# Performance work log

Measured on AMD Instinct MI355X. Metric: run time of the kernel, lower is better.

The kernel has to match this reference:

```python
import jax, jax.numpy as jnp
import numpy as np

B, N, D, H = 1024, 128, 256, 8
DH = D // H
CLIP = 10.0   # tanh clipping of logits (Kool attention model default)
NEG = -1e9    # mask value


def setup_inputs() -> dict:
    key = jax.random.key(0)
    ks = jax.random.split(key, 12)
    s = 1.0 / np.sqrt(D)
    rn = lambda k, shape, sc: jax.random.normal(k, shape, dtype=jnp.float32) * sc
    return {
        'coords': jax.random.uniform(ks[0], (B, N, 2), dtype=jnp.float32),
        'embeddings': rn(ks[1], (B, N, D), 1.0),
        'Wk': rn(ks[2], (D, D), s),            # glimpse key projection
        'Wv': rn(ks[3], (D, D), s),            # glimpse value projection
        'Wlk': rn(ks[4], (D, D), s),           # logit key projection
        'Wo': rn(ks[5], (D, D), s),            # glimpse output projection
        'Wc': rn(ks[6], (D, D), s),            # project_fixed_context
        'Ws': rn(ks[7], (2 * D, D), s),        # project_step_context (concat first,prev)
        'W_placeholder': rn(ks[8], (2 * D,), 1.0),  # first-step context placeholder
        'W1': rn(ks[9], (D, D), s),            # new_weight_1 (xavier-ish)
        'b1': jnp.zeros((D,), jnp.float32),    # new_bias_1 (init 0)
        'W2': jnp.zeros((D, D), jnp.float32),  # new_weight_2 (init 0 -> identity residual)
        'b2': jnp.zeros((D,), jnp.float32),    # new_bias_2 (init 0)
    }


def _decode(embeddings, Wk, Wv, Wlk, Wo, Wc, Ws, W_placeholder, W1, b1, W2, b2):
    Bq, Nq, Dq = embeddings.shape
    # precompute attention node data (fixed across steps)
    Kh = (embeddings @ Wk).reshape(Bq, Nq, H, DH).transpose(0, 2, 1, 3)  # [B,H,N,DH]
    Vh = (embeddings @ Wv).reshape(Bq, Nq, H, DH).transpose(0, 2, 1, 3)  # [B,H,N,DH]
    logitK = embeddings @ Wlk                                            # [B,N,D]
    glimpse0 = embeddings.mean(1)                                        # [B,D]
    visited0 = jnp.zeros((Bq, Nq), dtype=bool)
    idx0 = jnp.zeros((Bq,), dtype=jnp.int32)

    def body(carry, step):
        visited, first, prev, glimpse = carry
        first_emb = jnp.take_along_axis(embeddings, first[:, None, None], axis=1)[:, 0]
        prev_emb = jnp.take_along_axis(embeddings, prev[:, None, None], axis=1)[:, 0]
        step_ctx = jnp.where(step == 0,
                             jnp.broadcast_to(W_placeholder, (Bq, 2 * Dq)),
                             jnp.concatenate([first_emb, prev_emb], axis=-1))
        # query = graph context (updated glimpse) + step context
        q = glimpse @ Wc + step_ctx @ Ws                                  # [B,D]
        # query_transform: residual 2-layer MLP
        q = q + (jax.nn.relu(q @ W1 + b1) @ W2 + b2)
        # one_to_many_logits: MHA glimpse, then single-head pointer logits
        qh = q.reshape(Bq, H, DH)
        compat = jnp.einsum('bhd,bhnd->bhn', qh, Kh) / np.sqrt(DH)
        compat = jnp.where(visited[:, None, :], NEG, compat)
        attn = jax.nn.softmax(compat, axis=-1)
        heads = jnp.einsum('bhn,bhnd->bhd', attn, Vh).reshape(Bq, Dq)
        new_glimpse = heads @ Wo                                          # [B,D]
        logits = jnp.einsum('bd,bnd->bn', new_glimpse, logitK) / np.sqrt(Dq)
        logits = CLIP * jnp.tanh(logits)
        logits = jnp.where(visited, NEG, logits)
        log_p = jax.nn.log_softmax(logits, axis=-1)                       # [B,N]
        sel = jnp.argmax(log_p, axis=-1).astype(jnp.int32)                # greedy select
        visited = visited | jax.nn.one_hot(sel, Nq, dtype=bool)
        first = jnp.where(step == 0, sel, first)
        return (visited, first, sel, new_glimpse), (log_p, sel)

    _, (log_ps, sels) = jax.lax.scan(body, (visited0, idx0, idx0, glimpse0),
                                     jnp.arange(Nq))
    return log_ps.transpose(1, 0, 2), sels.transpose(1, 0)  # [B,steps,N], [B,steps]


def _tour_cost(coords, pi):
    route = jnp.take_along_axis(coords, pi[:, :, None].astype(jnp.int32), axis=1)  # [B,N,2]
    diffs = route - jnp.roll(route, -1, axis=1)
    return jnp.sqrt((diffs * diffs).sum(-1)).sum(-1)  # [B]


def reference(coords, embeddings, Wk, Wv, Wlk, Wo, Wc, Ws, W_placeholder, W1, b1, W2, b2):
    log_ps, pi = _decode(embeddings, Wk, Wv, Wlk, Wo, Wc, Ws, W_placeholder, W1, b1, W2, b2)
    cost = _tour_cost(coords, pi)
    ll = jnp.take_along_axis(log_ps, pi[:, :, None], axis=2)[:, :, 0].sum(-1)  # [B]
    return cost, ll
```

## Files before the change

kernel.cpp:

```cpp
#include <hip/hip_runtime.h>
#include <math.h>


#define BB 1024
#define NN 128
#define DD 256
#define HH 8

__device__ __forceinline__ float4 f4z() { return make_float4(0.f, 0.f, 0.f, 0.f); }
__device__ __forceinline__ float4 f4fma(float4 a, float4 b, float4 c) {
  c.x = fmaf(a.x, b.x, c.x); c.y = fmaf(a.y, b.y, c.y);
  c.z = fmaf(a.z, b.z, c.z); c.w = fmaf(a.w, b.w, c.w); return c;
}
__device__ __forceinline__ float4 svfma(float s, float4 w, float4 c) {
  c.x = fmaf(s, w.x, c.x); c.y = fmaf(s, w.y, c.y);
  c.z = fmaf(s, w.z, c.z); c.w = fmaf(s, w.w, c.w); return c;
}
__device__ __forceinline__ float4 f4scale(float4 a, float s) {
  a.x *= s; a.y *= s; a.z *= s; a.w *= s; return a;
}

#define WAVE_SYNC() do { asm volatile("s_waitcnt lgkmcnt(0)" ::: "memory"); \
                         __builtin_amdgcn_sched_barrier(0); } while (0)

__global__ void k_mean(const float* __restrict__ E, float* __restrict__ g0) {
  int b = blockIdx.x, t = threadIdx.x;
  const float* e = E + (size_t)b * NN * DD + t;
  float s = 0.f;
#pragma unroll 8
  for (int n = 0; n < NN; ++n) s += e[n * DD];
  g0[b * DD + t] = s * (1.f / 128.f);
}

__global__ void k_transpose(const float* __restrict__ A, float* __restrict__ AT) {
  __shared__ float tile[32][33];
  int bi = blockIdx.x & 7, bo = blockIdx.x >> 3;
  int tx = threadIdx.x & 31, ty = threadIdx.x >> 5;
  for (int j = 0; j < 32; j += 8)
    tile[ty + j][tx] = A[(size_t)(bi * 32 + ty + j) * DD + bo * 32 + tx];
  __syncthreads();
  for (int j = 0; j < 32; j += 8)
    AT[(size_t)(bo * 32 + ty + j) * DD + bi * 32 + tx] = tile[tx][ty + j];
}

__global__ __launch_bounds__(256) void k_gemm(const float* __restrict__ A,
                                              const float* __restrict__ Bm,
                                              float* __restrict__ C,
                                              int M, int Nn, int K, int transB) {
  __shared__ float As[32][33], Bs[32][33];
  int tn = blockIdx.x, tm = blockIdx.y;
  int t = threadIdx.x;
  int c = t & 31, r4 = t >> 5;
  float acc[4] = {0.f, 0.f, 0.f, 0.f};
  for (int k0 = 0; k0 < K; k0 += 32) {
#pragma unroll
    for (int i = 0; i < 4; ++i) {
      int li = t + i * 256; int ar = li >> 5, ac = li & 31;
      As[ar][ac] = A[(size_t)(tm * 32 + ar) * K + k0 + ac];
    }
    if (!transB) {
#pragma unroll
      for (int i = 0; i < 4; ++i) {
        int li = t + i * 256; int kk = li >> 5, cc = li & 31;
        Bs[kk][cc] = Bm[(size_t)(k0 + kk) * Nn + tn * 32 + cc];
      }
    } else {
#pragma unroll
      for (int i = 0; i < 4; ++i) {
        int li = t + i * 256; int cc = li >> 5, kk = li & 31;
        Bs[kk][cc] = Bm[(size_t)(tn * 32 + cc) * K + k0 + kk];
      }
    }
    __syncthreads();
#pragma unroll
    for (int kk = 0; kk < 32; ++kk) {
      float bv = Bs[kk][c];
#pragma unroll
      for (int i = 0; i < 4; ++i) acc[i] += As[r4 + i * 8][kk] * bv;
    }
    __syncthreads();
  }
#pragma unroll
  for (int i = 0; i < 4; ++i)
    C[(size_t)(tm * 32 + r4 + i * 8) * Nn + tn * 32 + c] = acc[i];
}

__global__ __launch_bounds__(512, 2) void k_decode(
    const float* __restrict__ E, const float* __restrict__ coords,
    const float* __restrict__ Ws, const float* __restrict__ W1,
    const float* __restrict__ b1, const float* __restrict__ W2,
    const float* __restrict__ b2, const float* __restrict__ WkT,
    const float* __restrict__ Wv, const float* __restrict__ M1,
    const float* __restrict__ M2, const float* __restrict__ Wph,
    const float* __restrict__ qlin0, float* __restrict__ out) {
  __shared__ float ctxS[512 * 4];
  __shared__ float qS[256 * 4];
  __shared__ float hS[256 * 4];
  __shared__ float q2S[256 * 4];
  __shared__ float headsS[256 * 4];
  __shared__ float qkS[8320];
  __shared__ float hEnS[8320];
  __shared__ float qlinS[4][256];
  __shared__ float gl2S[4][256];
  __shared__ float plS[4 * 2 * 8 * 8];
  __shared__ float alS[4 * 2 * 8];
  __shared__ float mlS[4 * 2 * 8 * 2];
  __shared__ int   lstS[4][128];
  __shared__ float logitS[4][128];
  __shared__ unsigned visS[4][4];
  __shared__ int   fpS[4][2];
  __shared__ float stS[4][8];

  const int t = threadIdx.x;
  const int w = t >> 6, l = t & 63;
  const int blk = blockIdx.x;
  const int ks = w;
  const int c0 = l * 4;
  const int fbb = w >> 1, w2 = w & 1;

  if (t < 256) {
    int bb = t >> 6, cc = (t & 63) * 4;
    *(float4*)&qlinS[bb][cc] =
        *(const float4*)(qlin0 + (size_t)(blk * 4 + bb) * DD + cc);
  }
  if (t < 16) visS[t >> 2][t & 3] = 0u;
  if (t < 4) {
    fpS[t][0] = 0; fpS[t][1] = 0;
#pragma unroll
    for (int j = 0; j < 8; ++j) stS[t][j] = 0.f;
  }
  __syncthreads();

  for (int step = 0; step < NN; ++step) {
    const int cnt = NN - step;

    if (step == 0) {
      float v = Wph[t];
      *(float4*)&ctxS[t * 4] = make_float4(v, v, v, v);
    } else {
      int bb = t >> 7, i4 = (t & 127) * 4;
      int node = (i4 < 256) ? fpS[bb][0] : fpS[bb][1];
      float4 v = *(const float4*)(E + (size_t)(blk * 4 + bb) * (NN * DD) +
                                  (size_t)node * DD + (i4 & 255));
      ctxS[(i4 + 0) * 4 + bb] = v.x; ctxS[(i4 + 1) * 4 + bb] = v.y;
      ctxS[(i4 + 2) * 4 + bb] = v.z; ctxS[(i4 + 3) * 4 + bb] = v.w;
    }
    __syncthreads();

    {
      float4 a0 = f4z(), a1 = f4z(), a2 = f4z(), a3 = f4z();
      const float* wp = Ws + (size_t)(ks * 64) * DD + c0;
      const float* cp = ctxS + (ks * 64) * 4;
#pragma unroll 8
      for (int k = 0; k < 64; ++k) {
        float4 wv = *(const float4*)wp; wp += DD;
        float4 cv = *(const float4*)cp; cp += 4;
        a0 = svfma(cv.x, wv, a0); a1 = svfma(cv.y, wv, a1);
        a2 = svfma(cv.z, wv, a2); a3 = svfma(cv.w, wv, a3);
      }
      *(float4*)&hEnS[ks * 1024 + 0 * 256 + c0] = a0;
      *(float4*)&hEnS[ks * 1024 + 1 * 256 + c0] = a1;
      *(float4*)&hEnS[ks * 1024 + 2 * 256 + c0] = a2;
      *(float4*)&hEnS[ks * 1024 + 3 * 256 + c0] = a3;
    }
    __syncthreads();
    {
      int bb = t & 3, cb = t >> 2;
#pragma unroll
      for (int it = 0; it < 2; ++it) {
        int c = cb + it * 128;
        float s = qlinS[bb][c];
#pragma unroll
        for (int sl = 0; sl < 8; ++sl) s += hEnS[sl * 1024 + bb * 256 + c];
        qS[c * 4 + bb] = s;
      }
    }
    __syncthreads();

    {
      float4 a0 = f4z(), a1 = f4z(), a2 = f4z(), a3 = f4z();
      const float* wp = W1 + (size_t)(ks * 32) * DD + c0;
      const float* qp = qS + (ks * 32) * 4;
#pragma unroll 8
      for (int k = 0; k < 32; ++k) {
        float4 wv = *(const float4*)wp; wp += DD;
        float4 qv = *(const float4*)qp; qp += 4;
        a0 = svfma(qv.x, wv, a0); a1 = svfma(qv.y, wv, a1);
        a2 = svfma(qv.z, wv, a2); a3 = svfma(qv.w, wv, a3);
      }
      *(float4*)&hEnS[ks * 1024 + 0 * 256 + c0] = a0;
      *(float4*)&hEnS[ks * 1024 + 1 * 256 + c0] = a1;
      *(float4*)&hEnS[ks * 1024 + 2 * 256 + c0] = a2;
      *(float4*)&hEnS[ks * 1024 + 3 * 256 + c0] = a3;
    }
    __syncthreads();
    {
      int bb = t & 3, cb = t >> 2;
#pragma unroll
      for (int it = 0; it < 2; ++it) {
        int c = cb + it * 128;
        float s = b1[c];
#pragma unroll
        for (int sl = 0; sl < 8; ++sl) s += hEnS[sl * 1024 + bb * 256 + c];
        hS[c * 4 + bb] = fmaxf(s, 0.f);
      }
    }
    __syncthreads();

    {
      float4 a0 = f4z(), a1 = f4z(), a2 = f4z(), a3 = f4z();
      const float* wp = W2 + (size_t)(ks * 32) * DD + c0;
      const float* hp = hS + (ks * 32) * 4;
#pragma unroll 8
      for (int k = 0; k < 32; ++k) {
        float4 wv = *(const float4*)wp; wp += DD;
        float4 hv = *(const float4*)hp; hp += 4;
        a0 = svfma(hv.x, wv, a0); a1 = svfma(hv.y, wv, a1);
        a2 = svfma(hv.z, wv, a2); a3 = svfma(hv.w, wv, a3);
      }
      *(float4*)&hEnS[ks * 1024 + 0 * 256 + c0] = a0;
      *(float4*)&hEnS[ks * 1024 + 1 * 256 + c0] = a1;
      *(float4*)&hEnS[ks * 1024 + 2 * 256 + c0] = a2;
      *(float4*)&hEnS[ks * 1024 + 3 * 256 + c0] = a3;
    }
    __syncthreads();
    {
      int bb = t & 3, cb = t >> 2;
#pragma unroll
      for (int it = 0; it < 2; ++it) {
        int c = cb + it * 128;
        float s = qS[c * 4 + bb] + b2[c];
#pragma unroll
        for (int sl = 0; sl < 8; ++sl) s += hEnS[sl * 1024 + bb * 256 + c];
        q2S[c * 4 + bb] = s;
      }
    }
    __syncthreads();

    {
      const int h = w;
      float4 a0 = f4z(), a1 = f4z(), a2 = f4z(), a3 = f4z();
      const float* wp = WkT + (size_t)(h * 32) * DD + c0;
      const float* qp = q2S + (h * 32) * 4;
#pragma unroll 8
      for (int k = 0; k < 32; ++k) {
        float4 wv = *(const float4*)wp; wp += DD;
        float4 qv = *(const float4*)qp; qp += 4;
        a0 = svfma(qv.x, wv, a0); a1 = svfma(qv.y, wv, a1);
        a2 = svfma(qv.z, wv, a2); a3 = svfma(qv.w, wv, a3);
      }
      *(float4*)&qkS[0 * 2080 + h * 260 + c0] = a0;
      *(float4*)&qkS[1 * 2080 + h * 260 + c0] = a1;
      *(float4*)&qkS[2 * 2080 + h * 260 + c0] = a2;
      *(float4*)&qkS[3 * 2080 + h * 260 + c0] = a3;
    }
    __syncthreads();

    {
      int bb = t >> 7, n = t & 127, half = (t >> 6) & 1;
      unsigned wd = visS[bb][n >> 5];
      bool unv = !((wd >> (n & 31)) & 1u);
      unsigned long long m = __ballot(unv);
      int rank = __popcll(m & ((1ull << l) - 1ull));
      int base = half ? (__popc(~visS[bb][0]) + __popc(~visS[bb][1])) : 0;
      if (unv) lstS[bb][base + rank] = n;
    }
    __syncthreads();

    const float* Eb = E + (size_t)(blk * 4 + fbb) * (NN * DD);
    float4 qr[8];
    {
      int h = l >> 3, s8 = l & 7;
#pragma unroll
      for (int j = 0; j < 8; ++j)
        qr[j] = *(float4*)&qkS[fbb * 2080 + h * 260 + s8 * 32 + j * 4];
    }
    __syncthreads();

    float4 hE[8];
#pragma unroll
    for (int i = 0; i < 8; ++i) hE[i] = f4z();
    float m_run = -INFINITY, l_run = 0.f;
    const int nA = (cnt + 1) >> 1;
    const int wstart = w2 ? nA : 0;
    const int wcount = w2 ? (cnt - nA) : nA;
    const int ntl = (wcount + 7) >> 3;
    const int slot = (fbb * 2 + w2) * 8;

    for (int tl = 0; tl < ntl; ++tl) {
      int rem = wcount - tl * 8;
      float pc[8];
      {
        int s8 = l & 7;
#pragma unroll
        for (int r = 0; r < 8; ++r) {
          int idx = wstart + tl * 8 + r;
          int row = lstS[fbb][(r < rem) ? idx : wstart];
          const float* ep = Eb + row * DD + s8 * 32;
          float4 acc = f4z();
#pragma unroll
          for (int j = 0; j < 8; ++j)
            acc = f4fma(*(const float4*)(ep + j * 4), qr[j], acc);
          pc[r] = (acc.x + acc.y) + (acc.z + acc.w);
        }
#pragma unroll
        for (int r = 0; r < 8; ++r) {
          pc[r] += __shfl_xor(pc[r], 1);
          pc[r] += __shfl_xor(pc[r], 2);
          pc[r] += __shfl_xor(pc[r], 4);
          pc[r] = (r < rem) ? pc[r] * 0.17677669529663687f : -INFINITY;
        }
      }
      float mt = pc[0];
#pragma unroll
      for (int r = 1; r < 8; ++r) mt = fmaxf(mt, pc[r]);
      float newm = fmaxf(m_run, mt);
      float alpha = expf(m_run - newm);
      float p[8], psum = 0.f;
#pragma unroll
      for (int r = 0; r < 8; ++r) { p[r] = expf(pc[r] - newm); psum += p[r]; }
      l_run = l_run * alpha + psum;
      m_run = newm;
      {
        int h = l >> 3;
        if ((l & 7) == 0) {
#pragma unroll
          for (int r = 0; r < 8; ++r) plS[(slot + r) * 8 + h] = p[r];
          alS[slot + h] = alpha;
        }
      }
      WAVE_SYNC();
      {
        float al[8];
#pragma unroll
        for (int h = 0; h < 8; ++h) al[h] = alS[slot + h];
#pragma unroll
        for (int h = 0; h < 8; ++h) hE[h] = f4scale(hE[h], al[h]);
        for (int r = 0; r < 8; ++r) {
          int idx = wstart + tl * 8 + r;
          int row = lstS[fbb][(r < rem) ? idx : wstart];
          float4 e4 = *(const float4*)(Eb + row * DD + l * 4);
          float4 p0 = *(float4*)&plS[(slot + r) * 8 + 0];
          float4 p1 = *(float4*)&plS[(slot + r) * 8 + 4];
          hE[0] = svfma(p0.x, e4, hE[0]); hE[1] = svfma(p0.y, e4, hE[1]);
          hE[2] = svfma(p0.z, e4, hE[2]); hE[3] = svfma(p0.w, e4, hE[3]);
          hE[4] = svfma(p1.x, e4, hE[4]); hE[5] = svfma(p1.y, e4, hE[5]);
          hE[6] = svfma(p1.z, e4, hE[6]); hE[7] = svfma(p1.w, e4, hE[7]);
        }
      }
      WAVE_SYNC();
    }
    {
      int h = l >> 3;
      if ((l & 7) == 0) {
        mlS[(slot + h) * 2 + 0] = m_run;
        mlS[(slot + h) * 2 + 1] = l_run;
      }
    }
    if (w2 == 1) {
#pragma unroll
      for (int h = 0; h < 8; ++h)
        *(float4*)&qkS[fbb * 2080 + h * 260 + l * 4] = hE[h];
    }
    __syncthreads();
    if (w2 == 0) {
      int sa = (fbb * 2 + 0) * 8, sb = (fbb * 2 + 1) * 8;
#pragma unroll
      for (int h = 0; h < 8; ++h) {
        float mA = mlS[(sa + h) * 2], lA = mlS[(sa + h) * 2 + 1];
        float mB = mlS[(sb + h) * 2], lB = mlS[(sb + h) * 2 + 1];
        float mm = fmaxf(mA, mB);
        float aA = expf(mA - mm), aB = expf(mB - mm);
        float lt = lA * aA + lB * aB;
        float4 vB = *(float4*)&qkS[fbb * 2080 + h * 260 + l * 4];
        float4 v;
        v.x = (hE[h].x * aA + vB.x * aB) / lt;
        v.y = (hE[h].y * aA + vB.y * aB) / lt;
        v.z = (hE[h].z * aA + vB.z * aB) / lt;
        v.w = (hE[h].w * aA + vB.w * aB) / lt;
        int dbase = h * 260 + l * 4;
        hEnS[(dbase + 0) * 4 + fbb] = v.x; hEnS[(dbase + 1) * 4 + fbb] = v.y;
        hEnS[(dbase + 2) * 4 + fbb] = v.z; hEnS[(dbase + 3) * 4 + fbb] = v.w;
      }
    }
    __syncthreads();

    {
      const int h = l >> 3;
      float4 a0 = f4z(), a1 = f4z(), a2 = f4z(), a3 = f4z();
      const float* wp = Wv + (size_t)(ks * 32) * DD + c0;
#pragma unroll 8
      for (int k = 0; k < 32; ++k) {
        float4 wv = *(const float4*)wp; wp += DD;
        float4 hv = *(float4*)&hEnS[(h * 260 + ks * 32 + k) * 4];
        a0 = svfma(hv.x, wv, a0); a1 = svfma(hv.y, wv, a1);
        a2 = svfma(hv.z, wv, a2); a3 = svfma(hv.w, wv, a3);
      }
      *(float4*)&qkS[ks * 1024 + 0 * 256 + c0] = a0;
      *(float4*)&qkS[ks * 1024 + 1 * 256 + c0] = a1;
      *(float4*)&qkS[ks * 1024 + 2 * 256 + c0] = a2;
      *(float4*)&qkS[ks * 1024 + 3 * 256 + c0] = a3;
    }
    __syncthreads();
    {
      int bb = t & 3, cb = t >> 2;
#pragma unroll
      for (int it = 0; it < 2; ++it) {
        int c = cb + it * 128;
        float s = 0.f;
#pragma unroll
        for (int sl = 0; sl < 8; ++sl) s += qkS[sl * 1024 + bb * 256 + c];
        headsS[c * 4 + bb] = s;
      }
    }
    __syncthreads();

    {
      float4 x0 = f4z(), x1 = f4z(), x2 = f4z(), x3 = f4z();
      float4 y0 = f4z(), y1 = f4z(), y2 = f4z(), y3 = f4z();
      const float* p1 = M1 + (size_t)(ks * 32) * DD + c0;
      const float* p2 = M2 + (size_t)(ks * 32) * DD + c0;
      const float* hp = headsS + (ks * 32) * 4;
#pragma unroll 4
      for (int k = 0; k < 32; ++k) {
        float4 w1v = *(const float4*)p1; p1 += DD;
        float4 w2v = *(const float4*)p2; p2 += DD;
        float4 hv = *(const float4*)hp; hp += 4;
        x0 = svfma(hv.x, w1v, x0); x1 = svfma(hv.y, w1v, x1);
        x2 = svfma(hv.z, w1v, x2); x3 = svfma(hv.w, w1v, x3);
        y0 = svfma(hv.x, w2v, y0); y1 = svfma(hv.y, w2v, y1);
        y2 = svfma(hv.z, w2v, y2); y3 = svfma(hv.w, w2v, y3);
      }
      *(float4*)&qkS[ks * 1024 + 0 * 256 + c0] = x0;
      *(float4*)&qkS[ks * 1024 + 1 * 256 + c0] = x1;
      *(float4*)&qkS[ks * 1024 + 2 * 256 + c0] = x2;
      *(float4*)&qkS[ks * 1024 + 3 * 256 + c0] = x3;
      *(float4*)&hEnS[ks * 1024 + 0 * 256 + c0] = y0;
      *(float4*)&hEnS[ks * 1024 + 1 * 256 + c0] = y1;
      *(float4*)&hEnS[ks * 1024 + 2 * 256 + c0] = y2;
      *(float4*)&hEnS[ks * 1024 + 3 * 256 + c0] = y3;
    }
    __syncthreads();
    {
      int bb = t & 3, cb = t >> 2;
#pragma unroll
      for (int it = 0; it < 2; ++it) {
        int c = cb + it * 128;
        float s1 = 0.f, s2 = 0.f;
#pragma unroll
        for (int sl = 0; sl < 8; ++sl) {
          s1 += qkS[sl * 1024 + bb * 256 + c];
          s2 += hEnS[sl * 1024 + bb * 256 + c];
        }
        qlinS[bb][c] = s1;
        gl2S[bb][c] = s2;
      }
    }
    __syncthreads();

    {
      int sbb = t >> 7, rid = (t & 127) >> 3, seg = t & 7;
      const float* Es = E + (size_t)(blk * 4 + sbb) * (NN * DD);
      const float* gp = &gl2S[sbb][seg * 32];
      int chunks = (cnt + 15) >> 4;
      for (int ch = 0; ch < chunks; ++ch) {
        int idx = ch * 16 + rid;
        bool val = idx < cnt;
        int row = lstS[sbb][val ? idx : 0];
        const float* ep = Es + row * DD + seg * 32;
        float4 acc = f4z();
#pragma unroll
        for (int j = 0; j < 8; ++j)
          acc = f4fma(*(const float4*)(ep + j * 4),
                      *(const float4*)(gp + j * 4), acc);
        float s = (acc.x + acc.y) + (acc.z + acc.w);
        s += __shfl_xor(s, 1);
        s += __shfl_xor(s, 2);
        s += __shfl_xor(s, 4);
        if (val && seg == 0) logitS[sbb][idx] = 10.f * tanhf(s * 0.0625f);
      }
    }
    __syncthreads();
    if (w2 == 0) {
      float v0 = (l < cnt) ? logitS[fbb][l] : -INFINITY;
      float v1 = (l + 64 < cnt) ? logitS[fbb][l + 64] : -INFINITY;
      float bv; int bi;
      if (v1 > v0) { bv = v1; bi = l + 64; } else { bv = v0; bi = l; }
#pragma unroll
      for (int off = 32; off >= 1; off >>= 1) {
        float ov = __shfl_xor(bv, off);
        int oi = __shfl_xor(bi, off);
        if (ov > bv || (ov == bv && oi < bi)) { bv = ov; bi = oi; }
      }
      float p0 = (l < cnt) ? expf(v0 - bv) : 0.f;
      float p1 = (l + 64 < cnt) ? expf(v1 - bv) : 0.f;
      float s = p0 + p1;
#pragma unroll
      for (int off = 32; off >= 1; off >>= 1) s += __shfl_xor(s, off);
      if (l == 0) {
        int sel = lstS[fbb][bi];
        float logp = -logf(s);
        visS[fbb][sel >> 5] |= (1u << (sel & 31));
        int gb = blk * 4 + fbb;
        float cx = coords[(size_t)gb * 256 + sel * 2];
        float cy = coords[(size_t)gb * 256 + sel * 2 + 1];
        stS[fbb][0] += logp;
        if (step == 0) {
          fpS[fbb][0] = sel; stS[fbb][2] = cx; stS[fbb][3] = cy;
        } else {
          float dx = stS[fbb][4] - cx, dy = stS[fbb][5] - cy;
          stS[fbb][1] += sqrtf(dx * dx + dy * dy);
        }
        fpS[fbb][1] = sel; stS[fbb][4] = cx; stS[fbb][5] = cy;
        if (step == NN - 1) {
          float dx = cx - stS[fbb][2], dy = cy - stS[fbb][3];
          out[gb] = stS[fbb][1] + sqrtf(dx * dx + dy * dy);
          out[BB + gb] = stS[fbb][0];
        }
      }
    }
    __syncthreads();
  }
}

extern "C" void kernel_launch(void* const* d_in, const int* in_sizes, int n_in,
                              void* d_out, int out_size, void* d_ws, size_t ws_size,
                              hipStream_t stream) {
  const float* coords = (const float*)d_in[0];
  const float* E      = (const float*)d_in[1];
  const float* Wk     = (const float*)d_in[2];
  const float* Wv     = (const float*)d_in[3];
  const float* Wlk    = (const float*)d_in[4];
  const float* Wo     = (const float*)d_in[5];
  const float* Wc     = (const float*)d_in[6];
  const float* Ws     = (const float*)d_in[7];
  const float* Wph    = (const float*)d_in[8];
  const float* W1     = (const float*)d_in[9];
  const float* b1     = (const float*)d_in[10];
  const float* W2     = (const float*)d_in[11];
  const float* b2     = (const float*)d_in[12];
  float* out = (float*)d_out;

  float* w = (float*)d_ws;
  float* g0    = w;
  float* qlin0 = g0 + (size_t)BB * DD;
  float* WkT   = qlin0 + (size_t)BB * DD;
  float* M1    = WkT + DD * DD;
  float* M2    = M1 + DD * DD;

  k_mean<<<BB, 256, 0, stream>>>(E, g0);
  k_transpose<<<64, 256, 0, stream>>>(Wk, WkT);
  k_gemm<<<dim3(8, 8), 256, 0, stream>>>(Wo, Wc, M1, 256, 256, 256, 0);
  k_gemm<<<dim3(8, 8), 256, 0, stream>>>(Wo, Wlk, M2, 256, 256, 256, 1);
  k_gemm<<<dim3(8, 32), 256, 0, stream>>>(g0, Wc, qlin0, 1024, 256, 256, 0);
  k_decode<<<256, 512, 0, stream>>>(E, coords, Ws, W1, b1, W2, b2, WkT, Wv,
                                    M1, M2, Wph, qlin0, out);
}
```

Measured before the change: 13.42 ms.

## Restructure decode kernel to 1024 threads with cached first-node projection

Rewrites the per-step decode loop to use 1024 threads per block, with a new thread-to-work mapping for each projection. The step-context projection is split into first and previous halves. The first-node half is computed once at step 0 and cached, and the placeholder projection is precomputed by a small kernel. The attention pass now uses one wave per (batch, head-pair) with a simpler online softmax and no cross-wave merge. The aim is to halve the Ws work per step and raise parallelism, at the cost of more shared memory and a larger block that may limit occupancy.

```diff
diff --git a/kernel.cpp b/kernel.cpp
--- a/kernel.cpp
+++ b/kernel.cpp
@@ -19,9 +19,6 @@
 __device__ __forceinline__ float4 f4scale(float4 a, float s) {
   a.x *= s; a.y *= s; a.z *= s; a.w *= s; return a;
 }
-
-#define WAVE_SYNC() do { asm volatile("s_waitcnt lgkmcnt(0)" ::: "memory"); \
-                         __builtin_amdgcn_sched_barrier(0); } while (0)
 
 __global__ void k_mean(const float* __restrict__ E, float* __restrict__ g0) {
   int b = blockIdx.x, t = threadIdx.x;
@@ -85,405 +82,271 @@
     C[(size_t)(tm * 32 + r4 + i * 8) * Nn + tn * 32 + c] = acc[i];
 }
 
-__global__ __launch_bounds__(512, 2) void k_decode(
+__global__ void k_qws0(const float* __restrict__ Wph, const float* __restrict__ Ws,
+                       float* __restrict__ qws0) {
+  int c = threadIdx.x;
+  float s = 0.f;
+  for (int k = 0; k < 512; ++k) s += Wph[k] * Ws[(size_t)k * DD + c];
+  qws0[c] = s;
+}
+
+__global__ __launch_bounds__(1024) void k_decode(
     const float* __restrict__ E, const float* __restrict__ coords,
     const float* __restrict__ Ws, const float* __restrict__ W1,
     const float* __restrict__ b1, const float* __restrict__ W2,
     const float* __restrict__ b2, const float* __restrict__ WkT,
     const float* __restrict__ Wv, const float* __restrict__ M1,
-    const float* __restrict__ M2, const float* __restrict__ Wph,
+    const float* __restrict__ M2, const float* __restrict__ qws0,
     const float* __restrict__ qlin0, float* __restrict__ out) {
-  __shared__ float ctxS[512 * 4];
-  __shared__ float qS[256 * 4];
-  __shared__ float hS[256 * 4];
-  __shared__ float q2S[256 * 4];
-  __shared__ float headsS[256 * 4];
+  __shared__ float qlinS[4][256];
+  __shared__ float gl2S[4][256];
+  __shared__ float qS[4][256];
+  __shared__ float hS[4][256];
+  __shared__ float q2S[4][256];
+  __shared__ float headsS[4][256];
+  __shared__ float qfS[4][256];
+  __shared__ float qpS[4][256];
+  __shared__ float P1[4096];
+  __shared__ float P2[4096];
   __shared__ float qkS[8320];
   __shared__ float hEnS[8320];
-  __shared__ float qlinS[4][256];
-  __shared__ float gl2S[4][256];
-  __shared__ float plS[4 * 2 * 8 * 8];
-  __shared__ float alS[4 * 2 * 8];
-  __shared__ float mlS[4 * 2 * 8 * 2];
   __shared__ int   lstS[4][128];
   __shared__ float logitS[4][128];
   __shared__ unsigned visS[4][4];
-  __shared__ int   fpS[4][2];
-  __shared__ float stS[4][8];
+  __shared__ int   selS[4];
+  __shared__ float stS[4][6];
 
   const int t = threadIdx.x;
   const int w = t >> 6, l = t & 63;
   const int blk = blockIdx.x;
-  const int ks = w;
+  const int gbb = w & 3;
+  const int gks = w >> 2;
   const int c0 = l * 4;
-  const int fbb = w >> 1, w2 = w & 1;
-
-  if (t < 256) {
-    int bb = t >> 6, cc = (t & 63) * 4;
-    *(float4*)&qlinS[bb][cc] =
-        *(const float4*)(qlin0 + (size_t)(blk * 4 + bb) * DD + cc);
-  }
+  const int cbb = t >> 8, cc = t & 255;
+
+  qlinS[cbb][cc] = qlin0[(size_t)(blk * 4 + cbb) * DD + cc];
   if (t < 16) visS[t >> 2][t & 3] = 0u;
   if (t < 4) {
-    fpS[t][0] = 0; fpS[t][1] = 0;
-#pragma unroll
-    for (int j = 0; j < 8; ++j) stS[t][j] = 0.f;
+#pragma unroll
+    for (int j = 0; j < 6; ++j) stS[t][j] = 0.f;
   }
   __syncthreads();
 
   for (int step = 0; step < NN; ++step) {
     const int cnt = NN - step;
 
-    if (step == 0) {
-      float v = Wph[t];
-      *(float4*)&ctxS[t * 4] = make_float4(v, v, v, v);
-    } else {
-      int bb = t >> 7, i4 = (t & 127) * 4;
-      int node = (i4 < 256) ? fpS[bb][0] : fpS[bb][1];
-      float4 v = *(const float4*)(E + (size_t)(blk * 4 + bb) * (NN * DD) +
-                                  (size_t)node * DD + (i4 & 255));
-      ctxS[(i4 + 0) * 4 + bb] = v.x; ctxS[(i4 + 1) * 4 + bb] = v.y;
-      ctxS[(i4 + 2) * 4 + bb] = v.z; ctxS[(i4 + 3) * 4 + bb] = v.w;
-    }
-    __syncthreads();
-
-    {
-      float4 a0 = f4z(), a1 = f4z(), a2 = f4z(), a3 = f4z();
-      const float* wp = Ws + (size_t)(ks * 64) * DD + c0;
-      const float* cp = ctxS + (ks * 64) * 4;
-#pragma unroll 8
-      for (int k = 0; k < 64; ++k) {
-        float4 wv = *(const float4*)wp; wp += DD;
-        float4 cv = *(const float4*)cp; cp += 4;
-        a0 = svfma(cv.x, wv, a0); a1 = svfma(cv.y, wv, a1);
-        a2 = svfma(cv.z, wv, a2); a3 = svfma(cv.w, wv, a3);
-      }
-      *(float4*)&hEnS[ks * 1024 + 0 * 256 + c0] = a0;
-      *(float4*)&hEnS[ks * 1024 + 1 * 256 + c0] = a1;
-      *(float4*)&hEnS[ks * 1024 + 2 * 256 + c0] = a2;
-      *(float4*)&hEnS[ks * 1024 + 3 * 256 + c0] = a3;
-    }
-    __syncthreads();
-    {
-      int bb = t & 3, cb = t >> 2;
-#pragma unroll
-      for (int it = 0; it < 2; ++it) {
-        int c = cb + it * 128;
-        float s = qlinS[bb][c];
-#pragma unroll
-        for (int sl = 0; sl < 8; ++sl) s += hEnS[sl * 1024 + bb * 256 + c];
-        qS[c * 4 + bb] = s;
-      }
-    }
-    __syncthreads();
-
-    {
-      float4 a0 = f4z(), a1 = f4z(), a2 = f4z(), a3 = f4z();
-      const float* wp = W1 + (size_t)(ks * 32) * DD + c0;
-      const float* qp = qS + (ks * 32) * 4;
-#pragma unroll 8
-      for (int k = 0; k < 32; ++k) {
-        float4 wv = *(const float4*)wp; wp += DD;
-        float4 qv = *(const float4*)qp; qp += 4;
-        a0 = svfma(qv.x, wv, a0); a1 = svfma(qv.y, wv, a1);
-        a2 = svfma(qv.z, wv, a2); a3 = svfma(qv.w, wv, a3);
-      }
-      *(float4*)&hEnS[ks * 1024 + 0 * 256 + c0] = a0;
-      *(float4*)&hEnS[ks * 1024 + 1 * 256 + c0] = a1;
-      *(float4*)&hEnS[ks * 1024 + 2 * 256 + c0] = a2;
-      *(float4*)&hEnS[ks * 1024 + 3 * 256 + c0] = a3;
-    }
-    __syncthreads();
-    {
-      int bb = t & 3, cb = t >> 2;
-#pragma unroll
-      for (int it = 0; it < 2; ++it) {
-        int c = cb + it * 128;
-        float s = b1[c];
-#pragma unroll
-        for (int sl = 0; sl < 8; ++sl) s += hEnS[sl * 1024 + bb * 256 + c];
-        hS[c * 4 + bb] = fmaxf(s, 0.f);
-      }
-    }
-    __syncthreads();
-
-    {
-      float4 a0 = f4z(), a1 = f4z(), a2 = f4z(), a3 = f4z();
-      const float* wp = W2 + (size_t)(ks * 32) * DD + c0;
-      const float* hp = hS + (ks * 32) * 4;
-#pragma unroll 8
-      for (int k = 0; k < 32; ++k) {
-        float4 wv = *(const float4*)wp; wp += DD;
-        float4 hv = *(const float4*)hp; hp += 4;
-        a0 = svfma(hv.x, wv, a0); a1 = svfma(hv.y, wv, a1);
-        a2 = svfma(hv.z, wv, a2); a3 = svfma(hv.w, wv, a3);
-      }
-      *(float4*)&hEnS[ks * 1024 + 0 * 256 + c0] = a0;
-      *(float4*)&hEnS[ks * 1024 + 1 * 256 + c0] = a1;
-      *(float4*)&hEnS[ks * 1024 + 2 * 256 + c0] = a2;
-      *(float4*)&hEnS[ks * 1024 + 3 * 256 + c0] = a3;
-    }
-    __syncthreads();
-    {
-      int bb = t & 3, cb = t >> 2;
-#pragma unroll
-      for (int it = 0; it < 2; ++it) {
-        int c = cb + it * 128;
-        float s = qS[c * 4 + bb] + b2[c];
-#pragma unroll
-        for (int sl = 0; sl < 8; ++sl) s += hEnS[sl * 1024 + bb * 256 + c];
-        q2S[c * 4 + bb] = s;
-      }
-    }
-    __syncthreads();
-
-    {
-      const int h = w;
-      float4 a0 = f4z(), a1 = f4z(), a2 = f4z(), a3 = f4z();
-      const float* wp = WkT + (size_t)(h * 32) * DD + c0;
-      const float* qp = q2S + (h * 32) * 4;
-#pragma unroll 8
-      for (int k = 0; k < 32; ++k) {
-        float4 wv = *(const float4*)wp; wp += DD;
-        float4 qv = *(const float4*)qp; qp += 4;
-        a0 = svfma(qv.x, wv, a0); a1 = svfma(qv.y, wv, a1);
-        a2 = svfma(qv.z, wv, a2); a3 = svfma(qv.w, wv, a3);
-      }
-      *(float4*)&qkS[0 * 2080 + h * 260 + c0] = a0;
-      *(float4*)&qkS[1 * 2080 + h * 260 + c0] = a1;
-      *(float4*)&qkS[2 * 2080 + h * 260 + c0] = a2;
-      *(float4*)&qkS[3 * 2080 + h * 260 + c0] = a3;
-    }
-    __syncthreads();
-
-    {
-      int bb = t >> 7, n = t & 127, half = (t >> 6) & 1;
+    {
+      float q = qlinS[cbb][cc];
+      q += (step == 0) ? qws0[cc] : (qfS[cbb][cc] + qpS[cbb][cc]);
+      qS[cbb][cc] = q;
+    }
+    if (t < 512) {
+      int bb = t >> 7, n = t & 127;
       unsigned wd = visS[bb][n >> 5];
       bool unv = !((wd >> (n & 31)) & 1u);
       unsigned long long m = __ballot(unv);
       int rank = __popcll(m & ((1ull << l) - 1ull));
-      int base = half ? (__popc(~visS[bb][0]) + __popc(~visS[bb][1])) : 0;
-      if (unv) lstS[bb][base + rank] = n;
-    }
-    __syncthreads();
-
-    const float* Eb = E + (size_t)(blk * 4 + fbb) * (NN * DD);
-    float4 qr[8];
-    {
-      int h = l >> 3, s8 = l & 7;
-#pragma unroll
-      for (int j = 0; j < 8; ++j)
-        qr[j] = *(float4*)&qkS[fbb * 2080 + h * 260 + s8 * 32 + j * 4];
-    }
-    __syncthreads();
-
-    float4 hE[8];
-#pragma unroll
-    for (int i = 0; i < 8; ++i) hE[i] = f4z();
-    float m_run = -INFINITY, l_run = 0.f;
-    const int nA = (cnt + 1) >> 1;
-    const int wstart = w2 ? nA : 0;
-    const int wcount = w2 ? (cnt - nA) : nA;
-    const int ntl = (wcount + 7) >> 3;
-    const int slot = (fbb * 2 + w2) * 8;
-
-    for (int tl = 0; tl < ntl; ++tl) {
-      int rem = wcount - tl * 8;
-      float pc[8];
-      {
-        int s8 = l & 7;
-#pragma unroll
-        for (int r = 0; r < 8; ++r) {
-          int idx = wstart + tl * 8 + r;
-          int row = lstS[fbb][(r < rem) ? idx : wstart];
-          const float* ep = Eb + row * DD + s8 * 32;
-          float4 acc = f4z();
-#pragma unroll
-          for (int j = 0; j < 8; ++j)
-            acc = f4fma(*(const float4*)(ep + j * 4), qr[j], acc);
-          pc[r] = (acc.x + acc.y) + (acc.z + acc.w);
-        }
-#pragma unroll
-        for (int r = 0; r < 8; ++r) {
-          pc[r] += __shfl_xor(pc[r], 1);
-          pc[r] += __shfl_xor(pc[r], 2);
-          pc[r] += __shfl_xor(pc[r], 4);
-          pc[r] = (r < rem) ? pc[r] * 0.17677669529663687f : -INFINITY;
-        }
-      }
-      float mt = pc[0];
-#pragma unroll
-      for (int r = 1; r < 8; ++r) mt = fmaxf(mt, pc[r]);
-      float newm = fmaxf(m_run, mt);
-      float alpha = expf(m_run - newm);
-      float p[8], psum = 0.f;
-#pragma unroll
-      for (int r = 0; r < 8; ++r) { p[r] = expf(pc[r] - newm); psum += p[r]; }
-      l_run = l_run * alpha + psum;
-      m_run = newm;
-      {
-        int h = l >> 3;
-        if ((l & 7) == 0) {
-#pragma unroll
-          for (int r = 0; r < 8; ++r) plS[(slot + r) * 8 + h] = p[r];
-          alS[slot + h] = alpha;
-        }
-      }
-      WAVE_SYNC();
-      {
-        float al[8];
-#pragma unroll
-        for (int h = 0; h < 8; ++h) al[h] = alS[slot + h];
-#pragma unroll
-        for (int h = 0; h < 8; ++h) hE[h] = f4scale(hE[h], al[h]);
-        for (int r = 0; r < 8; ++r) {
-          int idx = wstart + tl * 8 + r;
-          int row = lstS[fbb][(r < rem) ? idx : wstart];
-          float4 e4 = *(const float4*)(Eb + row * DD + l * 4);
-          float4 p0 = *(float4*)&plS[(slot + r) * 8 + 0];
-          float4 p1 = *(float4*)&plS[(slot + r) * 8 + 4];
-          hE[0] = svfma(p0.x, e4, hE[0]); hE[1] = svfma(p0.y, e4, hE[1]);
-          hE[2] = svfma(p0.z, e4, hE[2]); hE[3] = svfma(p0.w, e4, hE[3]);
-          hE[4] = svfma(p1.x, e4, hE[4]); hE[5] = svfma(p1.y, e4, hE[5]);
-          hE[6] = svfma(p1.z, e4, hE[6]); hE[7] = svfma(p1.w, e4, hE[7]);
-        }
-      }
-      WAVE_SYNC();
-    }
-    {
-      int h = l >> 3;
-      if ((l & 7) == 0) {
-        mlS[(slot + h) * 2 + 0] = m_run;
-        mlS[(slot + h) * 2 + 1] = l_run;
-      }
-    }
-    if (w2 == 1) {
-#pragma unroll
-      for (int h = 0; h < 8; ++h)
-        *(float4*)&qkS[fbb * 2080 + h * 260 + l * 4] = hE[h];
-    }
-    __syncthreads();
-    if (w2 == 0) {
-      int sa = (fbb * 2 + 0) * 8, sb = (fbb * 2 + 1) * 8;
-#pragma unroll
-      for (int h = 0; h < 8; ++h) {
-        float mA = mlS[(sa + h) * 2], lA = mlS[(sa + h) * 2 + 1];
-        float mB = mlS[(sb + h) * 2], lB = mlS[(sb + h) * 2 + 1];
-        float mm = fmaxf(mA, mB);
-        float aA = expf(mA - mm), aB = expf(mB - mm);
-        float lt = lA * aA + lB * aB;
-        float4 vB = *(float4*)&qkS[fbb * 2080 + h * 260 + l * 4];
-        float4 v;
-        v.x = (hE[h].x * aA + vB.x * aB) / lt;
-        v.y = (hE[h].y * aA + vB.y * aB) / lt;
-        v.z = (hE[h].z * aA + vB.z * aB) / lt;
-        v.w = (hE[h].w * aA + vB.w * aB) / lt;
-        int dbase = h * 260 + l * 4;
-        hEnS[(dbase + 0) * 4 + fbb] = v.x; hEnS[(dbase + 1) * 4 + fbb] = v.y;
-        hEnS[(dbase + 2) * 4 + fbb] = v.z; hEnS[(dbase + 3) * 4 + fbb] = v.w;
-      }
-    }
-    __syncthreads();
-
-    {
-      const int h = l >> 3;
-      float4 a0 = f4z(), a1 = f4z(), a2 = f4z(), a3 = f4z();
-      const float* wp = Wv + (size_t)(ks * 32) * DD + c0;
-#pragma unroll 8
-      for (int k = 0; k < 32; ++k) {
+      int half = (t >> 6) & 1;
+      int base2 = half ? (__popc(~visS[bb][0]) + __popc(~visS[bb][1])) : 0;
+      if (unv) lstS[bb][base2 + rank] = n;
+    }
+    __syncthreads();
+
+    {
+      float4 acc = f4z();
+      const float* wp = W1 + (size_t)(gks * 64) * DD + c0;
+      const float* xr = &qS[gbb][gks * 64];
+#pragma unroll 8
+      for (int k = 0; k < 64; ++k) {
         float4 wv = *(const float4*)wp; wp += DD;
-        float4 hv = *(float4*)&hEnS[(h * 260 + ks * 32 + k) * 4];
-        a0 = svfma(hv.x, wv, a0); a1 = svfma(hv.y, wv, a1);
-        a2 = svfma(hv.z, wv, a2); a3 = svfma(hv.w, wv, a3);
-      }
-      *(float4*)&qkS[ks * 1024 + 0 * 256 + c0] = a0;
-      *(float4*)&qkS[ks * 1024 + 1 * 256 + c0] = a1;
-      *(float4*)&qkS[ks * 1024 + 2 * 256 + c0] = a2;
-      *(float4*)&qkS[ks * 1024 + 3 * 256 + c0] = a3;
-    }
-    __syncthreads();
-    {
-      int bb = t & 3, cb = t >> 2;
-#pragma unroll
-      for (int it = 0; it < 2; ++it) {
-        int c = cb + it * 128;
-        float s = 0.f;
-#pragma unroll
-        for (int sl = 0; sl < 8; ++sl) s += qkS[sl * 1024 + bb * 256 + c];
-        headsS[c * 4 + bb] = s;
-      }
-    }
-    __syncthreads();
-
-    {
-      float4 x0 = f4z(), x1 = f4z(), x2 = f4z(), x3 = f4z();
-      float4 y0 = f4z(), y1 = f4z(), y2 = f4z(), y3 = f4z();
-      const float* p1 = M1 + (size_t)(ks * 32) * DD + c0;
-      const float* p2 = M2 + (size_t)(ks * 32) * DD + c0;
-      const float* hp = headsS + (ks * 32) * 4;
+        acc = svfma(xr[k], wv, acc);
+      }
+      *(float4*)&P1[(gks * 4 + gbb) * 256 + c0] = acc;
+    }
+    __syncthreads();
+    {
+      float s = b1[cc];
+#pragma unroll
+      for (int ks = 0; ks < 4; ++ks) s += P1[(ks * 4 + cbb) * 256 + cc];
+      hS[cbb][cc] = fmaxf(s, 0.f);
+    }
+    __syncthreads();
+
+    {
+      float4 acc = f4z();
+      const float* wp = W2 + (size_t)(gks * 64) * DD + c0;
+      const float* xr = &hS[gbb][gks * 64];
+#pragma unroll 8
+      for (int k = 0; k < 64; ++k) {
+        float4 wv = *(const float4*)wp; wp += DD;
+        acc = svfma(xr[k], wv, acc);
+      }
+      *(float4*)&P1[(gks * 4 + gbb) * 256 + c0] = acc;
+    }
+    __syncthreads();
+    {
+      float s = qS[cbb][cc] + b2[cc];
+#pragma unroll
+      for (int ks = 0; ks < 4; ++ks) s += P1[(ks * 4 + cbb) * 256 + cc];
+      q2S[cbb][cc] = s;
+    }
+    __syncthreads();
+
+    {
+#pragma unroll
+      for (int hh = 0; hh < 2; ++hh) {
+        int h = gks * 2 + hh;
+        float4 acc = f4z();
+        const float* wp = WkT + (size_t)(h * 32) * DD + c0;
+        const float* xr = &q2S[gbb][h * 32];
+#pragma unroll 8
+        for (int k = 0; k < 32; ++k) {
+          float4 wv = *(const float4*)wp; wp += DD;
+          acc = svfma(xr[k], wv, acc);
+        }
+        *(float4*)&qkS[(gbb * 8 + h) * 260 + c0] = acc;
+      }
+    }
+    __syncthreads();
+
+    {
+      const int hsel = l >> 5, s32 = l & 31;
+      const int fh = gks * 2 + hsel;
+      const float* qkp = &qkS[(gbb * 8 + fh) * 260 + s32 * 8];
+      float4 qr0 = *(const float4*)qkp, qr1 = *(const float4*)(qkp + 4);
+      const float* Eb = E + (size_t)(blk * 4 + gbb) * (NN * DD);
+      float4 hE0 = f4z(), hE1 = f4z();
+      float m_run = -INFINITY, l_run = 0.f;
+
+      for (int base = 0; base < cnt; base += 4) {
+        float4 e0[4], e1[4];
+        float pc[4];
+#pragma unroll
+        for (int r = 0; r < 4; ++r) {
+          int idx = base + r;
+          int ridx = (idx < cnt) ? idx : (cnt - 1);
+          int row = lstS[gbb][ridx];
+          const float* ep = Eb + row * DD + s32 * 8;
+          e0[r] = *(const float4*)ep;
+          e1[r] = *(const float4*)(ep + 4);
+        }
+#pragma unroll
+        for (int r = 0; r < 4; ++r) {
+          float4 a = f4fma(e0[r], qr0, f4z());
+          a = f4fma(e1[r], qr1, a);
+          float s = (a.x + a.y) + (a.z + a.w);
+          s += __shfl_xor(s, 1);
+          s += __shfl_xor(s, 2);
+          s += __shfl_xor(s, 4);
+          s += __shfl_xor(s, 8);
+          s += __shfl_xor(s, 16);
+          pc[r] = (base + r < cnt) ? s * 0.17677669529663687f : -INFINITY;
+        }
+        float mt = fmaxf(fmaxf(pc[0], pc[1]), fmaxf(pc[2], pc[3]));
+        float newm = fmaxf(m_run, mt);
+        float alpha = expf(m_run - newm);
+        float psum = 0.f;
+#pragma unroll
+        for (int r = 0; r < 4; ++r) { pc[r] = expf(pc[r] - newm); psum += pc[r]; }
+        l_run = l_run * alpha + psum;
+        m_run = newm;
+        hE0 = f4scale(hE0, alpha); hE1 = f4scale(hE1, alpha);
+#pragma unroll
+        for (int r = 0; r < 4; ++r) {
+          hE0 = svfma(pc[r], e0[r], hE0);
+          hE1 = svfma(pc[r], e1[r], hE1);
+        }
+      }
+      float inv = 1.f / l_run;
+      float* op = &hEnS[(gbb * 8 + fh) * 260 + s32 * 8];
+      *(float4*)op = f4scale(hE0, inv);
+      *(float4*)(op + 4) = f4scale(hE1, inv);
+    }
+    __syncthreads();
+
+    {
+      int hh = l >> 3;
+      const float* hrow = &hEnS[(gbb * 8 + hh) * 260 + gks * 64];
+      float4 acc = f4z();
+      const float* wp = Wv + (size_t)(gks * 64) * DD + c0;
+#pragma unroll 8
+      for (int k = 0; k < 64; ++k) {
+        float4 wv = *(const float4*)wp; wp += DD;
+        acc = svfma(hrow[k], wv, acc);
+      }
+      *(float4*)&P1[(gks * 4 + gbb) * 256 + c0] = acc;
+    }
+    __syncthreads();
+    {
+      float s = 0.f;
+#pragma unroll
+      for (int ks = 0; ks < 4; ++ks) s += P1[(ks * 4 + cbb) * 256 + cc];
+      headsS[cbb][cc] = s;
+    }
+    __syncthreads();
+
+    {
+      float4 a1 = f4z(), a2 = f4z();
+      const float* p1p = M1 + (size_t)(gks * 64) * DD + c0;
+      const float* p2p = M2 + (size_t)(gks * 64) * DD + c0;
+      const float* xr = &headsS[gbb][gks * 64];
 #pragma unroll 4
-      for (int k = 0; k < 32; ++k) {
-        float4 w1v = *(const float4*)p1; p1 += DD;
-        float4 w2v = *(const float4*)p2; p2 += DD;
-        float4 hv = *(const float4*)hp; hp += 4;
-        x0 = svfma(hv.x, w1v, x0); x1 = svfma(hv.y, w1v, x1);
-        x2 = svfma(hv.z, w1v, x2); x3 = svfma(hv.w, w1v, x3);
-        y0 = svfma(hv.x, w2v, y0); y1 = svfma(hv.y, w2v, y1);
-        y2 = svfma(hv.z, w2v, y2); y3 = svfma(hv.w, w2v, y3);
-      }
-      *(float4*)&qkS[ks * 1024 + 0 * 256 + c0] = x0;
-      *(float4*)&qkS[ks * 1024 + 1 * 256 + c0] = x1;
-      *(float4*)&qkS[ks * 1024 + 2 * 256 + c0] = x2;
-      *(float4*)&qkS[ks * 1024 + 3 * 256 + c0] = x3;
-      *(float4*)&hEnS[ks * 1024 + 0 * 256 + c0] = y0;
-      *(float4*)&hEnS[ks * 1024 + 1 * 256 + c0] = y1;
-      *(float4*)&hEnS[ks * 1024 + 2 * 256 + c0] = y2;
-      *(float4*)&hEnS[ks * 1024 + 3 * 256 + c0] = y3;
-    }
-    __syncthreads();
-    {
-      int bb = t & 3, cb = t >> 2;
-#pragma unroll
-      for (int it = 0; it < 2; ++it) {
-        int c = cb + it * 128;
-        float s1 = 0.f, s2 = 0.f;
-#pragma unroll
-        for (int sl = 0; sl < 8; ++sl) {
-          s1 += qkS[sl * 1024 + bb * 256 + c];
-          s2 += hEnS[sl * 1024 + bb * 256 + c];
-        }
-        qlinS[bb][c] = s1;
-        gl2S[bb][c] = s2;
-      }
-    }
-    __syncthreads();
-
-    {
-      int sbb = t >> 7, rid = (t & 127) >> 3, seg = t & 7;
-      const float* Es = E + (size_t)(blk * 4 + sbb) * (NN * DD);
-      const float* gp = &gl2S[sbb][seg * 32];
-      int chunks = (cnt + 15) >> 4;
-      for (int ch = 0; ch < chunks; ++ch) {
-        int idx = ch * 16 + rid;
-        bool val = idx < cnt;
-        int row = lstS[sbb][val ? idx : 0];
-        const float* ep = Es + row * DD + seg * 32;
-        float4 acc = f4z();
-#pragma unroll
-        for (int j = 0; j < 8; ++j)
-          acc = f4fma(*(const float4*)(ep + j * 4),
-                      *(const float4*)(gp + j * 4), acc);
-        float s = (acc.x + acc.y) + (acc.z + acc.w);
-        s += __shfl_xor(s, 1);
-        s += __shfl_xor(s, 2);
-        s += __shfl_xor(s, 4);
-        if (val && seg == 0) logitS[sbb][idx] = 10.f * tanhf(s * 0.0625f);
-      }
-    }
-    __syncthreads();
-    if (w2 == 0) {
-      float v0 = (l < cnt) ? logitS[fbb][l] : -INFINITY;
-      float v1 = (l + 64 < cnt) ? logitS[fbb][l + 64] : -INFINITY;
+      for (int k = 0; k < 64; ++k) {
+        float s = xr[k];
+        float4 w1v = *(const float4*)p1p; p1p += DD;
+        float4 w2v = *(const float4*)p2p; p2p += DD;
+        a1 = svfma(s, w1v, a1);
+        a2 = svfma(s, w2v, a2);
+      }
+      *(float4*)&P1[(gks * 4 + gbb) * 256 + c0] = a1;
+      *(float4*)&P2[(gks * 4 + gbb) * 256 + c0] = a2;
+    }
+    __syncthreads();
+    {
+      float s1 = 0.f, s2 = 0.f;
+#pragma unroll
+      for (int ks = 0; ks < 4; ++ks) {
+        s1 += P1[(ks * 4 + cbb) * 256 + cc];
+        s2 += P2[(ks * 4 + cbb) * 256 + cc];
+      }
+      qlinS[cbb][cc] = s1;
+      gl2S[cbb][cc] = s2;
+    }
+    __syncthreads();
+
+    {
+      const float* Eb = E + (size_t)(blk * 4 + gbb) * (NN * DD);
+      float4 gv = *(const float4*)&gl2S[gbb][c0];
+      for (int base = gks; base < cnt; base += 16) {
+        float sres[4];
+#pragma unroll
+        for (int j = 0; j < 4; ++j) {
+          int idx = base + j * 4;
+          int row = lstS[gbb][(idx < cnt) ? idx : 0];
+          float4 ev = *(const float4*)(Eb + row * DD + c0);
+          float4 a = f4fma(ev, gv, f4z());
+          sres[j] = (a.x + a.y) + (a.z + a.w);
+        }
+#pragma unroll
+        for (int j = 0; j < 4; ++j) {
+          float s = sres[j];
+          s += __shfl_xor(s, 1);
+          s += __shfl_xor(s, 2);
+          s += __shfl_xor(s, 4);
+          s += __shfl_xor(s, 8);
+          s += __shfl_xor(s, 16);
+          s += __shfl_xor(s, 32);
+          int idx = base + j * 4;
+          if (l == 0 && idx < cnt) logitS[gbb][idx] = 10.f * tanhf(s * 0.0625f);
+        }
+      }
+    }
+    __syncthreads();
+
+    if (w < 4) {
+      int bb = w;
+      float v0 = (l < cnt) ? logitS[bb][l] : -INFINITY;
+      float v1 = (l + 64 < cnt) ? logitS[bb][l + 64] : -INFINITY;
       float bv; int bi;
       if (v1 > v0) { bv = v1; bi = l + 64; } else { bv = v0; bi = l; }
 #pragma unroll
@@ -498,28 +361,70 @@
 #pragma unroll
       for (int off = 32; off >= 1; off >>= 1) s += __shfl_xor(s, off);
       if (l == 0) {
-        int sel = lstS[fbb][bi];
+        int sel = lstS[bb][bi];
         float logp = -logf(s);
-        visS[fbb][sel >> 5] |= (1u << (sel & 31));
-        int gb = blk * 4 + fbb;
-        float cx = coords[(size_t)gb * 256 + sel * 2];
-        float cy = coords[(size_t)gb * 256 + sel * 2 + 1];
-        stS[fbb][0] += logp;
+        visS[bb][sel >> 5] |= (1u << (sel & 31));
+        selS[bb] = sel;
+        int gb = blk * 4 + bb;
+        float cx = coords[(size_t)gb * (NN * 2) + sel * 2];
+        float cy = coords[(size_t)gb * (NN * 2) + sel * 2 + 1];
+        stS[bb][0] += logp;
         if (step == 0) {
-          fpS[fbb][0] = sel; stS[fbb][2] = cx; stS[fbb][3] = cy;
+          stS[bb][2] = cx; stS[bb][3] = cy;
         } else {
-          float dx = stS[fbb][4] - cx, dy = stS[fbb][5] - cy;
-          stS[fbb][1] += sqrtf(dx * dx + dy * dy);
-        }
-        fpS[fbb][1] = sel; stS[fbb][4] = cx; stS[fbb][5] = cy;
+          float dx = stS[bb][4] - cx, dy = stS[bb][5] - cy;
+          stS[bb][1] += sqrtf(dx * dx + dy * dy);
+        }
+        stS[bb][4] = cx; stS[bb][5] = cy;
         if (step == NN - 1) {
-          float dx = cx - stS[fbb][2], dy = cy - stS[fbb][3];
-          out[gb] = stS[fbb][1] + sqrtf(dx * dx + dy * dy);
-          out[BB + gb] = stS[fbb][0];
-        }
-      }
-    }
-    __syncthreads();
+          float dx = cx - stS[bb][2], dy = cy - stS[bb][3];
+          out[gb] = stS[bb][1] + sqrtf(dx * dx + dy * dy);
+          out[BB + gb] = stS[bb][0];
+        }
+      }
+    }
+    __syncthreads();
+
+    if (step + 1 < NN) {
+      qS[cbb][cc] = E[(size_t)(blk * 4 + cbb) * (NN * DD) +
+                      (size_t)selS[cbb] * DD + cc];
+      __syncthreads();
+      {
+        float4 acc = f4z();
+        const float* wp = Ws + (size_t)(256 + gks * 64) * DD + c0;
+        const float* xr = &qS[gbb][gks * 64];
+#pragma unroll 8
+        for (int k = 0; k < 64; ++k) {
+          float4 wv = *(const float4*)wp; wp += DD;
+          acc = svfma(xr[k], wv, acc);
+        }
+        *(float4*)&P1[(gks * 4 + gbb) * 256 + c0] = acc;
+        if (step == 0) {
+          float4 accF = f4z();
+          const float* wpF = Ws + (size_t)(gks * 64) * DD + c0;
+#pragma unroll 8
+          for (int k = 0; k < 64; ++k) {
+            float4 wv = *(const float4*)wpF; wpF += DD;
+            accF = svfma(xr[k], wv, accF);
+          }
+          *(float4*)&P2[(gks * 4 + gbb) * 256 + c0] = accF;
+        }
+      }
+      __syncthreads();
+      {
+        float s = 0.f;
+#pragma unroll
+        for (int ks = 0; ks < 4; ++ks) s += P1[(ks * 4 + cbb) * 256 + cc];
+        qpS[cbb][cc] = s;
+        if (step == 0) {
+          float sf = 0.f;
+#pragma unroll
+          for (int ks = 0; ks < 4; ++ks) sf += P2[(ks * 4 + cbb) * 256 + cc];
+          qfS[cbb][cc] = sf;
+        }
+      }
+      __syncthreads();
+    }
   }
 }
 
@@ -547,12 +452,14 @@
   float* WkT   = qlin0 + (size_t)BB * DD;
   float* M1    = WkT + DD * DD;
   float* M2    = M1 + DD * DD;
+  float* qws0  = M2 + DD * DD;
 
   k_mean<<<BB, 256, 0, stream>>>(E, g0);
   k_transpose<<<64, 256, 0, stream>>>(Wk, WkT);
   k_gemm<<<dim3(8, 8), 256, 0, stream>>>(Wo, Wc, M1, 256, 256, 256, 0);
   k_gemm<<<dim3(8, 8), 256, 0, stream>>>(Wo, Wlk, M2, 256, 256, 256, 1);
   k_gemm<<<dim3(8, 32), 256, 0, stream>>>(g0, Wc, qlin0, 1024, 256, 256, 0);
-  k_decode<<<256, 512, 0, stream>>>(E, coords, Ws, W1, b1, W2, b2, WkT, Wv,
-                                    M1, M2, Wph, qlin0, out);
-}
+  k_qws0<<<1, 256, 0, stream>>>(Wph, Ws, qws0);
+  k_decode<<<256, 1024, 0, stream>>>(E, coords, Ws, W1, b1, W2, b2, WkT, Wv,
+                                     M1, M2, qws0, qlin0, out);
+}
```

Result: slower. 18.71 ms (+39.4%).
